# Kernel optimization log

Hardware: AMD Instinct MI355X
Metric: run time of the kernel (lower is better)

The kernel has to match this reference:

```python
import math
import jax, jax.numpy as jnp
import numpy as np

B, S, M, D, H, FF = 2, 2048, 64, 1024, 16, 4096
HD = D // H


def setup_inputs() -> dict:
    key = jax.random.key(0)
    ks = jax.random.split(key, 16)
    w = lambda k, shape: jax.random.normal(k, shape, dtype=jnp.float32) * 0.02
    # RoPE angles: theta_i = pos / 10000^(2i/head_dim)
    inv_freq = 1.0 / (10000.0 ** (jnp.arange(0, HD, 2, dtype=jnp.float32) / HD))
    ang = jnp.arange(S, dtype=jnp.float32)[:, None] * inv_freq[None, :]  # (S, HD//2)
    return {
        "tgt": jax.random.normal(ks[0], (B, S, D), dtype=jnp.float32),
        "memory": jax.random.normal(ks[1], (B, M, D), dtype=jnp.float32),
        "rope_cos": jnp.cos(ang),
        "rope_sin": jnp.sin(ang),
        "W_qkv": w(ks[2], (D, 3 * D)), "b_qkv": jnp.zeros((3 * D,), jnp.float32),
        "W_o": w(ks[3], (D, D)), "b_o": jnp.zeros((D,), jnp.float32),
        "Wq_c": w(ks[4], (D, D)), "bq_c": jnp.zeros((D,), jnp.float32),
        "Wk_c": w(ks[5], (D, D)), "bk_c": jnp.zeros((D,), jnp.float32),
        "Wv_c": w(ks[6], (D, D)), "bv_c": jnp.zeros((D,), jnp.float32),
        "W_co": w(ks[7], (D, D)), "b_co": jnp.zeros((D,), jnp.float32),
        "W1": w(ks[8], (D, FF)), "b1": jnp.zeros((FF,), jnp.float32),
        "W2": w(ks[9], (FF, D)), "b2": jnp.zeros((D,), jnp.float32),
        "g1": jnp.ones((D,), jnp.float32), "be1": jnp.zeros((D,), jnp.float32),
        "g2": jnp.ones((D,), jnp.float32), "be2": jnp.zeros((D,), jnp.float32),
        "g3": jnp.ones((D,), jnp.float32), "be3": jnp.zeros((D,), jnp.float32),
    }


def _layer_norm(x, g, b, eps=1e-5):
    mu = jnp.mean(x, axis=-1, keepdims=True)
    var = jnp.mean(jnp.square(x - mu), axis=-1, keepdims=True)
    return (x - mu) * jax.lax.rsqrt(var + eps) * g + b


def _apply_rope(x, cos, sin):
    # x: (B, H, S, HD); cos/sin: (S, HD//2). Pairs (even, odd) rotated as complex.
    xe, xo = x[..., 0::2], x[..., 1::2]
    c = cos[None, None]
    s = sin[None, None]
    re = xe * c - xo * s
    im = xe * s + xo * c
    return jnp.stack([re, im], axis=-1).reshape(x.shape)


def reference(tgt, memory, rope_cos, rope_sin, W_qkv, b_qkv, W_o, b_o,
              Wq_c, bq_c, Wk_c, bk_c, Wv_c, bv_c, W_co, b_co,
              W1, b1, W2, b2, g1, be1, g2, be2, g3, be3):
    b, s, d = tgt.shape
    scale = 1.0 / math.sqrt(HD)

    # --- RoPE self-attention (causal) ---
    x = _layer_norm(tgt, g1, be1)
    qkv = (x @ W_qkv + b_qkv).reshape(b, s, 3, H, HD)
    qkv = jnp.transpose(qkv, (2, 0, 3, 1, 4))  # (3, b, H, s, HD)
    q, k, v = qkv[0], qkv[1], qkv[2]
    q = _apply_rope(q, rope_cos[:s], rope_sin[:s])
    k = _apply_rope(k, rope_cos[:s], rope_sin[:s])
    attn = jnp.einsum('bhqd,bhkd->bhqk', q, k) * scale
    causal = jnp.tril(jnp.ones((s, s), dtype=bool))
    attn = jnp.where(causal[None, None], attn, -1e9)
    attn = jax.nn.softmax(attn, axis=-1)
    sa = jnp.einsum('bhqk,bhkd->bhqd', attn, v)
    sa = jnp.transpose(sa, (0, 2, 1, 3)).reshape(b, s, d)
    tgt = tgt + (sa @ W_o + b_o)

    # --- cross-attention to memory (no positional encoding) ---
    x = _layer_norm(tgt, g2, be2)
    m = memory.shape[1]
    qc = (x @ Wq_c + bq_c).reshape(b, s, H, HD).transpose(0, 2, 1, 3)
    kc = (memory @ Wk_c + bk_c).reshape(b, m, H, HD).transpose(0, 2, 1, 3)
    vc = (memory @ Wv_c + bv_c).reshape(b, m, H, HD).transpose(0, 2, 1, 3)
    ca = jax.nn.softmax(jnp.einsum('bhqd,bhkd->bhqk', qc, kc) * scale, axis=-1)
    co = jnp.einsum('bhqk,bhkd->bhqd', ca, vc)
    co = jnp.transpose(co, (0, 2, 1, 3)).reshape(b, s, d)
    tgt = tgt + (co @ W_co + b_co)

    # --- FFN (exact GELU, dropout disabled = eval) ---
    x = _layer_norm(tgt, g3, be3)
    ffn = jax.nn.gelu(x @ W1 + b1, approximate=False) @ W2 + b2
    return tgt + ffn
```

## Files before the change

### kernel.cpp

```cpp
#include <hip/hip_runtime.h>

typedef unsigned short u16;
typedef short bf16x8 __attribute__((ext_vector_type(8)));
typedef float f32x4 __attribute__((ext_vector_type(4)));

#define HN 16
#define SD 64
#define SEQ 2048
#define DM 1024
#define QSC 0.18033688f

__device__ __forceinline__ float bf2f(u16 h) {
  return __uint_as_float(((unsigned int)h) << 16);
}
__device__ __forceinline__ u16 f2bf(float f) {
  unsigned int x = __float_as_uint(f);
  x += 0x7fffu + ((x >> 16) & 1u);
  return (u16)(x >> 16);
}
__device__ __forceinline__ float geluf(float x) {
  return 0.5f * x * (1.0f + erff(x * 0.70710678118654752f));
}
__device__ __forceinline__ void load_lds16(const u16* g, u16* l) {
  __builtin_amdgcn_global_load_lds(
      (const __attribute__((address_space(1))) void*)g,
      (__attribute__((address_space(3))) void*)l, 16, 0, 0);
}

__global__ __launch_bounds__(256) void transpose_f2b(
    const float* __restrict__ in, u16* __restrict__ out, int K, int N) {
  __shared__ u16 T[64][72];
  const int n0 = blockIdx.x * 64, k0 = blockIdx.y * 64;
  const int tid = threadIdx.x;
#pragma unroll
  for (int it = 0; it < 2; ++it) {
    const int t = it * 256 + tid, r = t >> 3, c = (t & 7) * 8;
    const float* src = &in[(size_t)(k0 + r) * N + n0 + c];
    float4 d0 = *(const float4*)src;
    float4 d1 = *(const float4*)(src + 4);
    T[r][c + 0] = f2bf(d0.x);
    T[r][c + 1] = f2bf(d0.y);
    T[r][c + 2] = f2bf(d0.z);
    T[r][c + 3] = f2bf(d0.w);
    T[r][c + 4] = f2bf(d1.x);
    T[r][c + 5] = f2bf(d1.y);
    T[r][c + 6] = f2bf(d1.z);
    T[r][c + 7] = f2bf(d1.w);
  }
  __syncthreads();
#pragma unroll
  for (int it = 0; it < 2; ++it) {
    const int t = it * 256 + tid, r = t >> 3, c = (t & 7) * 8;
    uint4 d;
    u16* p = (u16*)&d;
#pragma unroll
    for (int j = 0; j < 8; ++j) p[j] = T[c + j][r];
    *(uint4*)&out[(size_t)(n0 + r) * K + k0 + c] = d;
  }
}

__global__ __launch_bounds__(256) void f2b_kernel(const float* __restrict__ in,
                                                  u16* __restrict__ out) {
  const int i = (blockIdx.x * 256 + threadIdx.x) * 4;
  float4 d = *(const float4*)&in[i];
  uint2 o;
  u16* po = (u16*)&o;
  po[0] = f2bf(d.x);
  po[1] = f2bf(d.y);
  po[2] = f2bf(d.z);
  po[3] = f2bf(d.w);
  *(uint2*)&out[i] = o;
}

__global__ __launch_bounds__(256) void ln_kernel(
    const float* __restrict__ x, const float* __restrict__ g,
    const float* __restrict__ be, u16* __restrict__ y) {
  const int row = blockIdx.x, tid = threadIdx.x;
  const float* xr = x + (size_t)row * DM;
  float4 d = *(const float4*)&xr[tid * 4];
  float v[4] = {d.x, d.y, d.z, d.w};
  float s1 = 0.f, s2 = 0.f;
#pragma unroll
  for (int j = 0; j < 4; ++j) {
    s1 += v[j];
    s2 += v[j] * v[j];
  }
#pragma unroll
  for (int dd = 1; dd < 64; dd <<= 1) {
    s1 += __shfl_xor(s1, dd, 64);
    s2 += __shfl_xor(s2, dd, 64);
  }
  __shared__ float p1[4], p2[4];
  const int lane = tid & 63, wv = tid >> 6;
  if (lane == 0) {
    p1[wv] = s1;
    p2[wv] = s2;
  }
  __syncthreads();
  s1 = p1[0] + p1[1] + p1[2] + p1[3];
  s2 = p2[0] + p2[1] + p2[2] + p2[3];
  const float mu = s1 * (1.f / DM);
  const float rs = rsqrtf(fmaxf(s2 * (1.f / DM) - mu * mu, 0.f) + 1e-5f);
  float4 gg = *(const float4*)&g[tid * 4];
  float4 bb = *(const float4*)&be[tid * 4];
  const float gv[4] = {gg.x, gg.y, gg.z, gg.w};
  const float bv[4] = {bb.x, bb.y, bb.z, bb.w};
  uint2 o;
  u16* po = (u16*)&o;
#pragma unroll
  for (int j = 0; j < 4; ++j) po[j] = f2bf((v[j] - mu) * rs * gv[j] + bv[j]);
  *(uint2*)&y[(size_t)row * DM + tid * 4] = o;
}

__global__ __launch_bounds__(256) void rope_kernel(
    u16* __restrict__ q, u16* __restrict__ k, const float* __restrict__ ct,
    const float* __restrict__ st) {
  const long long NG = 2LL * HN * SEQ * 8;
  long long gidx = (long long)blockIdx.x * 256 + threadIdx.x;
  const bool isq = (gidx < NG);
  u16* p = isq ? q : k;
  const float m = isq ? QSC : 1.0f;
  long long gg = isq ? gidx : gidx - NG;
  const int pib = (int)(gg & 7) * 4;
  const int s = (int)((gg >> 3) & (SEQ - 1));
  uint4 d = *(uint4*)&p[gg * 8];
  u16* e = (u16*)&d;
#pragma unroll
  for (int j = 0; j < 4; ++j) {
    const float c = ct[s * 32 + pib + j];
    const float sn = st[s * 32 + pib + j];
    const float xe = bf2f(e[2 * j]), xo = bf2f(e[2 * j + 1]);
    e[2 * j] = f2bf((xe * c - xo * sn) * m);
    e[2 * j + 1] = f2bf((xe * sn + xo * c) * m);
  }
  *(uint4*)&p[gg * 8] = d;
}

template <int EPI, int TM>
__global__ __launch_bounds__(256) void gemm_bt(
    const u16* __restrict__ A, const u16* __restrict__ Bt,
    const float* __restrict__ bias, const float* __restrict__ resid,
    void* __restrict__ C0, u16* __restrict__ C1, u16* __restrict__ C2, int M,
    int N, int K, int rpbl, float sc) {
  constexpr int MI = TM / 32;
  __shared__ __align__(16) u16 As[TM][64];
  __shared__ __align__(16) u16 Bs[128][64];
  const int tid = threadIdx.x;
  const int lane = tid & 63, wv = tid >> 6;
  const int l16 = lane & 15, quad = lane >> 4;

  int bx = blockIdx.x, by = blockIdx.y;
  const int gx = gridDim.x, gy = gridDim.y;
  if ((gy & 7) == 0) {
    const int f = by * gx + bx;
    const int c = f & 7, j = f >> 3;
    const int jm = j / gx;
    by = c * (gy >> 3) + jm;
    bx = j - jm * gx;
  }
  const int m0 = by * TM, n0 = bx * 128;
  const int wm = (wv >> 1) * (TM / 2), wn = (wv & 1) * 64;

  const int srow = lane >> 3;
  const int sblk = (lane & 7) ^ srow;
  const u16* ag[MI];
  const u16* bg[4];
  u16* la[MI];
  u16* lb[4];
#pragma unroll
  for (int i = 0; i < MI; ++i) {
    const int r0 = i * 32 + wv * 8;
    ag[i] = A + (size_t)(m0 + r0 + srow) * K + sblk * 8;
    la[i] = &As[r0][0] + lane * 8;
  }
#pragma unroll
  for (int i = 0; i < 4; ++i) {
    const int r0 = i * 32 + wv * 8;
    bg[i] = Bt + (size_t)(n0 + r0 + srow) * K + sblk * 8;
    lb[i] = &Bs[r0][0] + lane * 8;
  }

  f32x4 acc[MI][4] = {};

  for (int k0 = 0; k0 < K; k0 += 64) {
    __syncthreads();
#pragma unroll
    for (int i = 0; i < MI; ++i) load_lds16(ag[i] + k0, la[i]);
#pragma unroll
    for (int i = 0; i < 4; ++i) load_lds16(bg[i] + k0, lb[i]);
    __syncthreads();
#pragma unroll
    for (int kk = 0; kk < 2; ++kk) {
      bf16x8 af[MI], bfr[4];
#pragma unroll
      for (int mi = 0; mi < MI; ++mi) {
        const int row = wm + mi * 16 + l16;
        const int blk = (kk * 4 + quad) ^ (row & 7);
        af[mi] = *(const bf16x8*)&As[row][blk * 8];
      }
#pragma unroll
      for (int ni = 0; ni < 4; ++ni) {
        const int row = wn + ni * 16 + l16;
        const int blk = (kk * 4 + quad) ^ (row & 7);
        bfr[ni] = *(const bf16x8*)&Bs[row][blk * 8];
      }
#pragma unroll
      for (int mi = 0; mi < MI; ++mi)
#pragma unroll
        for (int ni = 0; ni < 4; ++ni)
          acc[mi][ni] = __builtin_amdgcn_mfma_f32_16x16x32_bf16(
              af[mi], bfr[ni], acc[mi][ni], 0, 0, 0);
    }
  }

  const int SL = 1 << rpbl;
#pragma unroll
  for (int mi = 0; mi < MI; ++mi) {
#pragma unroll
    for (int ni = 0; ni < 4; ++ni) {
#pragma unroll
      for (int r = 0; r < 4; ++r) {
        const int row = m0 + wm + mi * 16 + quad * 4 + r;
        const int col = n0 + wn + ni * 16 + l16;
        float vv = acc[mi][ni][r] + bias[col];
        if (EPI == 1) {
          vv += resid[(size_t)row * N + col];
          ((float*)C0)[(size_t)row * N + col] = vv;
        } else if (EPI == 2) {
          ((u16*)C0)[(size_t)row * N + col] = f2bf(geluf(vv));
        } else if (EPI == 3) {
          const int which = col >> 10;
          const int nn = col & 1023;
          const int h = nn >> 6, hd = nn & 63;
          const int b = row >> rpbl;
          const int s = row & (SL - 1);
          if (which == 2) {
            C2[(((size_t)b * HN + h) * SD + hd) * SL + s] = f2bf(vv);
          } else {
            u16* o = (which == 0) ? (u16*)C0 : C1;
            o[(((size_t)b * HN + h) * SL + s) * SD + hd] = f2bf(vv);
          }
        } else if (EPI == 4) {
          vv *= sc;
          const int h = col >> 6, hd = col & 63;
          const int b = row >> rpbl;
          const int s = row & (SL - 1);
          ((u16*)C0)[(((size_t)b * HN + h) * SL + s) * SD + hd] = f2bf(vv);
        } else if (EPI == 5) {
          const int h = col >> 6, hd = col & 63;
          const int b = row >> rpbl;
          const int s = row & (SL - 1);
          ((u16*)C0)[(((size_t)b * HN + h) * SD + hd) * SL + s] = f2bf(vv);
        } else {
          ((u16*)C0)[(size_t)row * N + col] = f2bf(vv);
        }
      }
    }
  }
}

template <int CAUSAL>
__global__ __launch_bounds__(512, 4) void attn_kernel(
    const u16* __restrict__ q, const u16* __restrict__ k,
    const u16* __restrict__ vt, u16* __restrict__ out, int kv_len) {
  __shared__ u16 Qs[128][72], Ks[64][72], VTs[64][72];
  __shared__ u16 Ps[128][68];
  const int tid = threadIdx.x;
  const int lane = tid & 63, wv = tid >> 6;
  const int t2 = wv >> 2, w4 = wv & 3;
  const int l16 = lane & 15, quad = lane >> 4;
  const int bx = blockIdx.x, bh = blockIdx.y;
  const int qtA = bx;
  const int qtB = CAUSAL ? (31 - bx) : (bx + 16);
  const int qt = t2 ? qtB : qtA;
  const u16* qb = q + (size_t)bh * SEQ * SD;
  const u16* kb = k + (size_t)bh * kv_len * SD;
  const u16* vtb = vt + (size_t)bh * SD * kv_len;

#pragma unroll
  for (int it = 0; it < 2; ++it) {
    const int t = it * 512 + tid, r = t >> 3, c = (t & 7) * 8;
    const int qrow = (r < 64) ? (qtA * 64 + r) : (qtB * 64 + (r - 64));
    *(uint4*)&Qs[r][c] = *(const uint4*)&qb[(size_t)qrow * SD + c];
  }

  f32x4 o_acc[4] = {};
  float l_i[4] = {};

  const int ktiles = CAUSAL ? (qtB + 1) : ((kv_len + 63) >> 6);
  const int sr = tid >> 3, sc8 = (tid & 7) * 8;

  for (int kt = 0; kt < ktiles; ++kt) {
    const uint4 kd = *(const uint4*)&kb[((size_t)kt * 64 + sr) * SD + sc8];
    const uint4 vd = *(const uint4*)&vtb[(size_t)sr * kv_len + kt * 64 + sc8];
    __syncthreads();
    *(uint4*)&Ks[sr][sc8] = kd;
    *(uint4*)&VTs[sr][sc8] = vd;
    __syncthreads();

    if (kt <= qt) {
      const int roff = t2 * 64 + w4 * 16;
      f32x4 s_acc[4] = {};
#pragma unroll
      for (int kk = 0; kk < 64; kk += 32) {
        const bf16x8 aq = *(const bf16x8*)&Qs[roff + l16][kk + quad * 8];
#pragma unroll
        for (int ni = 0; ni < 4; ++ni) {
          const bf16x8 bk = *(const bf16x8*)&Ks[ni * 16 + l16][kk + quad * 8];
          s_acc[ni] = __builtin_amdgcn_mfma_f32_16x16x32_bf16(aq, bk, s_acc[ni],
                                                              0, 0, 0);
        }
      }
      float rsum[4] = {0.f, 0.f, 0.f, 0.f};
      const bool dg = CAUSAL && (kt == qt);
#pragma unroll
      for (int ni = 0; ni < 4; ++ni)
#pragma unroll
        for (int r = 0; r < 4; ++r) {
          float sv = s_acc[ni][r];
          if (dg && (ni * 16 + l16 > w4 * 16 + quad * 4 + r)) sv = -1e9f;
          const float pe = __builtin_amdgcn_exp2f(sv);
          rsum[r] += pe;
          Ps[wv * 16 + quad * 4 + r][ni * 16 + l16] =
              (u16)(__float_as_uint(pe) >> 16);
        }
#pragma unroll
      for (int r = 0; r < 4; ++r) {
#pragma unroll
        for (int dd = 1; dd < 16; dd <<= 1)
          rsum[r] += __shfl_xor(rsum[r], dd, 64);
        l_i[r] += rsum[r];
      }
#pragma unroll
      for (int kk = 0; kk < 64; kk += 32) {
        const bf16x8 ap = *(const bf16x8*)&Ps[wv * 16 + l16][kk + quad * 8];
#pragma unroll
        for (int ni = 0; ni < 4; ++ni) {
          const bf16x8 bv = *(const bf16x8*)&VTs[ni * 16 + l16][kk + quad * 8];
          o_acc[ni] = __builtin_amdgcn_mfma_f32_16x16x32_bf16(ap, bv, o_acc[ni],
                                                              0, 0, 0);
        }
      }
    }
  }

  const int b = bh >> 4, h = bh & 15;
#pragma unroll
  for (int r = 0; r < 4; ++r) {
    const float inv = 1.f / l_i[r];
    const int s = qt * 64 + w4 * 16 + quad * 4 + r;
#pragma unroll
    for (int ni = 0; ni < 4; ++ni)
      out[((size_t)b * SEQ + s) * DM + h * SD + ni * 16 + l16] =
          f2bf(o_acc[ni][r] * inv);
  }
}

extern "C" void kernel_launch(void* const* d_in, const int* in_sizes, int n_in,
                              void* d_out, int out_size, void* d_ws,
                              size_t ws_size, hipStream_t stream) {
  (void)in_sizes;
  (void)n_in;
  (void)out_size;
  (void)ws_size;
  const float* tgt = (const float*)d_in[0];
  const float* mem = (const float*)d_in[1];
  const float* rc = (const float*)d_in[2];
  const float* rsn = (const float*)d_in[3];
  const float* W_qkv = (const float*)d_in[4];
  const float* b_qkv = (const float*)d_in[5];
  const float* W_o = (const float*)d_in[6];
  const float* b_o = (const float*)d_in[7];
  const float* Wq_c = (const float*)d_in[8];
  const float* bq_c = (const float*)d_in[9];
  const float* Wk_c = (const float*)d_in[10];
  const float* bk_c = (const float*)d_in[11];
  const float* Wv_c = (const float*)d_in[12];
  const float* bv_c = (const float*)d_in[13];
  const float* W_co = (const float*)d_in[14];
  const float* b_co = (const float*)d_in[15];
  const float* W1 = (const float*)d_in[16];
  const float* b1 = (const float*)d_in[17];
  const float* W2 = (const float*)d_in[18];
  const float* b2 = (const float*)d_in[19];
  const float* g1 = (const float*)d_in[20];
  const float* be1 = (const float*)d_in[21];
  const float* g2 = (const float*)d_in[22];
  const float* be2 = (const float*)d_in[23];
  const float* g3 = (const float*)d_in[24];
  const float* be3 = (const float*)d_in[25];

  const size_t M1 = 1048576;
  u16* w = (u16*)d_ws;
  u16* WTqkv = w;
  u16* WTo = w + 3 * M1;
  u16* WTqc = w + 4 * M1;
  u16* WTkc = w + 5 * M1;
  u16* WTvc = w + 6 * M1;
  u16* WTco = w + 7 * M1;
  u16* WT1 = w;
  u16* WT2 = w + 4 * M1;
  u16* xb = w + 8 * M1;
  u16* qb = w + 12 * M1;
  u16* kb = w + 16 * M1;
  u16* vbT = w + 20 * M1;
  u16* at = w + 24 * M1;
  u16* kc = w + 28 * M1;
  u16* vcT = kc + 131072;
  u16* memb = vcT + 131072;
  u16* ffh = qb;
  float* res = (float*)d_out;

  dim3 blk(256), blk512(512);
  transpose_f2b<<<dim3(48, 16), blk, 0, stream>>>(W_qkv, WTqkv, 1024, 3072);
  transpose_f2b<<<dim3(16, 16), blk, 0, stream>>>(W_o, WTo, 1024, 1024);
  transpose_f2b<<<dim3(16, 16), blk, 0, stream>>>(Wq_c, WTqc, 1024, 1024);
  transpose_f2b<<<dim3(16, 16), blk, 0, stream>>>(Wk_c, WTkc, 1024, 1024);
  transpose_f2b<<<dim3(16, 16), blk, 0, stream>>>(Wv_c, WTvc, 1024, 1024);
  transpose_f2b<<<dim3(16, 16), blk, 0, stream>>>(W_co, WTco, 1024, 1024);
  f2b_kernel<<<128, blk, 0, stream>>>(mem, memb);

  ln_kernel<<<4096, blk, 0, stream>>>(tgt, g1, be1, xb);
  gemm_bt<3, 128><<<dim3(24, 32), blk, 0, stream>>>(
      xb, WTqkv, b_qkv, nullptr, qb, kb, vbT, 4096, 3072, 1024, 11, 1.f);
  rope_kernel<<<4096, blk, 0, stream>>>(qb, kb, rc, rsn);
  attn_kernel<1><<<dim3(16, 32), blk512, 0, stream>>>(qb, kb, vbT, at, 2048);
  gemm_bt<1, 64><<<dim3(8, 64), blk, 0, stream>>>(
      at, WTo, b_o, tgt, res, nullptr, nullptr, 4096, 1024, 1024, 0, 1.f);
  ln_kernel<<<4096, blk, 0, stream>>>(res, g2, be2, xb);
  gemm_bt<4, 64><<<dim3(8, 64), blk, 0, stream>>>(
      xb, WTqc, bq_c, nullptr, qb, nullptr, nullptr, 4096, 1024, 1024, 11, QSC);
  gemm_bt<4, 64><<<dim3(8, 2), blk, 0, stream>>>(
      memb, WTkc, bk_c, nullptr, kc, nullptr, nullptr, 128, 1024, 1024, 6, 1.f);
  gemm_bt<5, 64><<<dim3(8, 2), blk, 0, stream>>>(
      memb, WTvc, bv_c, nullptr, vcT, nullptr, nullptr, 128, 1024, 1024, 6,
      1.f);
  attn_kernel<0><<<dim3(16, 32), blk512, 0, stream>>>(qb, kc, vcT, at, 64);
  gemm_bt<1, 64><<<dim3(8, 64), blk, 0, stream>>>(
      at, WTco, b_co, res, res, nullptr, nullptr, 4096, 1024, 1024, 0, 1.f);
  transpose_f2b<<<dim3(64, 16), blk, 0, stream>>>(W1, WT1, 1024, 4096);
  transpose_f2b<<<dim3(16, 64), blk, 0, stream>>>(W2, WT2, 4096, 1024);
  ln_kernel<<<4096, blk, 0, stream>>>(res, g3, be3, xb);
  gemm_bt<2, 128><<<dim3(32, 32), blk, 0, stream>>>(
      xb, WT1, b1, nullptr, ffh, nullptr, nullptr, 4096, 4096, 1024, 0, 1.f);
  gemm_bt<1, 64><<<dim3(8, 64), blk, 0, stream>>>(
      ffh, WT2, b2, res, res, nullptr, nullptr, 4096, 1024, 4096, 0, 1.f);
}
```

Measured before the change: 534.8 us.

## Fuse weight prep launches, RoPE into QKV epilogue, and split-KV attention

Merges the weight transposes and the memory conversion into two batched prep kernels. RoPE and the Q scale move into the QKV GEMM epilogue through a lane shuffle, which removes the separate rope pass over q and k. The cross-attention K and V projections now share one launch via blockIdx.z. Attention is restructured so each block handles one 64-row query tile, with its two wave groups splitting the KV tiles and merging partial results through LDS. The aim is fewer launches, less memory traffic and more blocks for attention, at the cost of extra LDS traffic and synchronisation for the merge.

```diff
diff --git a/kernel.cpp b/kernel.cpp
--- a/kernel.cpp
+++ b/kernel.cpp
@@ -27,11 +27,11 @@
       (__attribute__((address_space(3))) void*)l, 16, 0, 0);
 }
 
-__global__ __launch_bounds__(256) void transpose_f2b(
-    const float* __restrict__ in, u16* __restrict__ out, int K, int N) {
-  __shared__ u16 T[64][72];
-  const int n0 = blockIdx.x * 64, k0 = blockIdx.y * 64;
-  const int tid = threadIdx.x;
+__device__ __forceinline__ void trans_tile(const float* __restrict__ in,
+                                           u16* __restrict__ out, int K, int N,
+                                           int tx, int ty, int tid,
+                                           u16 (*T)[72]) {
+  const int n0 = tx * 64, k0 = ty * 64;
 #pragma unroll
   for (int it = 0; it < 2; ++it) {
     const int t = it * 256 + tid, r = t >> 3, c = (t & 7) * 8;
@@ -59,17 +59,54 @@
   }
 }
 
-__global__ __launch_bounds__(256) void f2b_kernel(const float* __restrict__ in,
-                                                  u16* __restrict__ out) {
-  const int i = (blockIdx.x * 256 + threadIdx.x) * 4;
-  float4 d = *(const float4*)&in[i];
+__global__ __launch_bounds__(256) void prep1(
+    const float* __restrict__ Wqkv, const float* __restrict__ Wo,
+    const float* __restrict__ Wqc, const float* __restrict__ Wkc,
+    const float* __restrict__ Wvc, const float* __restrict__ Wco,
+    u16* __restrict__ Tqkv, u16* __restrict__ To, u16* __restrict__ Tqc,
+    u16* __restrict__ Tkc, u16* __restrict__ Tvc, u16* __restrict__ Tco,
+    const float* __restrict__ mem, u16* __restrict__ memb) {
+  __shared__ u16 T[64][72];
+  const int t = blockIdx.x, tid = threadIdx.x;
+  if (t < 768) {
+    trans_tile(Wqkv, Tqkv, 1024, 3072, t % 48, t / 48, tid, T);
+    return;
+  }
+  if (t < 2048) {
+    const int u = t - 768, m = u >> 8, sub = u & 255;
+    const float* in;
+    u16* out;
+    if (m == 0) { in = Wo; out = To; }
+    else if (m == 1) { in = Wqc; out = Tqc; }
+    else if (m == 2) { in = Wkc; out = Tkc; }
+    else if (m == 3) { in = Wvc; out = Tvc; }
+    else { in = Wco; out = Tco; }
+    trans_tile(in, out, 1024, 1024, sub & 15, sub >> 4, tid, T);
+    return;
+  }
+  const int i = ((t - 2048) * 256 + tid) * 4;
+  float4 d = *(const float4*)&mem[i];
   uint2 o;
   u16* po = (u16*)&o;
   po[0] = f2bf(d.x);
   po[1] = f2bf(d.y);
   po[2] = f2bf(d.z);
   po[3] = f2bf(d.w);
-  *(uint2*)&out[i] = o;
+  *(uint2*)&memb[i] = o;
+}
+
+__global__ __launch_bounds__(256) void prep2(const float* __restrict__ W1,
+                                             const float* __restrict__ W2,
+                                             u16* __restrict__ T1,
+                                             u16* __restrict__ T2) {
+  __shared__ u16 T[64][72];
+  const int t = blockIdx.x, tid = threadIdx.x;
+  if (t < 1024) {
+    trans_tile(W1, T1, 1024, 4096, t & 63, t >> 6, tid, T);
+  } else {
+    const int u = t - 1024;
+    trans_tile(W2, T2, 4096, 1024, u & 15, u >> 4, tid, T);
+  }
 }
 
 __global__ __launch_bounds__(256) void ln_kernel(
@@ -112,42 +149,24 @@
   *(uint2*)&y[(size_t)row * DM + tid * 4] = o;
 }
 
-__global__ __launch_bounds__(256) void rope_kernel(
-    u16* __restrict__ q, u16* __restrict__ k, const float* __restrict__ ct,
-    const float* __restrict__ st) {
-  const long long NG = 2LL * HN * SEQ * 8;
-  long long gidx = (long long)blockIdx.x * 256 + threadIdx.x;
-  const bool isq = (gidx < NG);
-  u16* p = isq ? q : k;
-  const float m = isq ? QSC : 1.0f;
-  long long gg = isq ? gidx : gidx - NG;
-  const int pib = (int)(gg & 7) * 4;
-  const int s = (int)((gg >> 3) & (SEQ - 1));
-  uint4 d = *(uint4*)&p[gg * 8];
-  u16* e = (u16*)&d;
-#pragma unroll
-  for (int j = 0; j < 4; ++j) {
-    const float c = ct[s * 32 + pib + j];
-    const float sn = st[s * 32 + pib + j];
-    const float xe = bf2f(e[2 * j]), xo = bf2f(e[2 * j + 1]);
-    e[2 * j] = f2bf((xe * c - xo * sn) * m);
-    e[2 * j + 1] = f2bf((xe * sn + xo * c) * m);
-  }
-  *(uint4*)&p[gg * 8] = d;
-}
-
 template <int EPI, int TM>
 __global__ __launch_bounds__(256) void gemm_bt(
     const u16* __restrict__ A, const u16* __restrict__ Bt,
     const float* __restrict__ bias, const float* __restrict__ resid,
     void* __restrict__ C0, u16* __restrict__ C1, u16* __restrict__ C2, int M,
-    int N, int K, int rpbl, float sc) {
+    int N, int K, int rpbl, float sc, const float* __restrict__ rcos,
+    const float* __restrict__ rsin) {
   constexpr int MI = TM / 32;
   __shared__ __align__(16) u16 As[TM][64];
   __shared__ __align__(16) u16 Bs[128][64];
   const int tid = threadIdx.x;
   const int lane = tid & 63, wv = tid >> 6;
   const int l16 = lane & 15, quad = lane >> 4;
+
+  if (EPI == 6 && blockIdx.z) {
+    Bt = (const u16*)C1;
+    bias = resid;
+  }
 
   int bx = blockIdx.x, by = blockIdx.y;
   const int gx = gridDim.x, gy = gridDim.y;
@@ -229,6 +248,7 @@
         } else if (EPI == 2) {
           ((u16*)C0)[(size_t)row * N + col] = f2bf(geluf(vv));
         } else if (EPI == 3) {
+          const float partner = __shfl_xor(vv, 1);
           const int which = col >> 10;
           const int nn = col & 1023;
           const int h = nn >> 6, hd = nn & 63;
@@ -237,8 +257,14 @@
           if (which == 2) {
             C2[(((size_t)b * HN + h) * SD + hd) * SL + s] = f2bf(vv);
           } else {
-            u16* o = (which == 0) ? (u16*)C0 : C1;
-            o[(((size_t)b * HN + h) * SL + s) * SD + hd] = f2bf(vv);
+            const int p = hd >> 1;
+            const float cv = rcos[s * 32 + p];
+            const float sv2 = rsin[s * 32 + p];
+            float o = (hd & 1) ? (partner * sv2 + vv * cv)
+                               : (vv * cv - partner * sv2);
+            if (which == 0) o *= QSC;
+            u16* dst = (which == 0) ? (u16*)C0 : C1;
+            dst[(((size_t)b * HN + h) * SL + s) * SD + hd] = f2bf(o);
           }
         } else if (EPI == 4) {
           vv *= sc;
@@ -251,6 +277,14 @@
           const int b = row >> rpbl;
           const int s = row & (SL - 1);
           ((u16*)C0)[(((size_t)b * HN + h) * SD + hd) * SL + s] = f2bf(vv);
+        } else if (EPI == 6) {
+          const int h = col >> 6, hd = col & 63;
+          const int b = row >> rpbl;
+          const int s = row & (SL - 1);
+          if (blockIdx.z == 0)
+            ((u16*)C0)[(((size_t)b * HN + h) * SL + s) * SD + hd] = f2bf(vv);
+          else
+            C2[(((size_t)b * HN + h) * SD + hd) * SL + s] = f2bf(vv);
         } else {
           ((u16*)C0)[(size_t)row * N + col] = f2bf(vv);
         }
@@ -263,56 +297,68 @@
 __global__ __launch_bounds__(512, 4) void attn_kernel(
     const u16* __restrict__ q, const u16* __restrict__ k,
     const u16* __restrict__ vt, u16* __restrict__ out, int kv_len) {
-  __shared__ u16 Qs[128][72], Ks[64][72], VTs[64][72];
+  __shared__ u16 Qs[64][72];
+  __shared__ u16 Ks[128][72];
+  __shared__ u16 VTs[64][136];
   __shared__ u16 Ps[128][68];
   const int tid = threadIdx.x;
   const int lane = tid & 63, wv = tid >> 6;
   const int t2 = wv >> 2, w4 = wv & 3;
   const int l16 = lane & 15, quad = lane >> 4;
-  const int bx = blockIdx.x, bh = blockIdx.y;
-  const int qtA = bx;
-  const int qtB = CAUSAL ? (31 - bx) : (bx + 16);
-  const int qt = t2 ? qtB : qtA;
-  const u16* qb = q + (size_t)bh * SEQ * SD;
+  const int qt = blockIdx.x, bh = blockIdx.y;
+  const u16* qb = q + ((size_t)bh * SEQ + qt * 64) * SD;
   const u16* kb = k + (size_t)bh * kv_len * SD;
   const u16* vtb = vt + (size_t)bh * SD * kv_len;
 
-#pragma unroll
-  for (int it = 0; it < 2; ++it) {
-    const int t = it * 512 + tid, r = t >> 3, c = (t & 7) * 8;
-    const int qrow = (r < 64) ? (qtA * 64 + r) : (qtB * 64 + (r - 64));
-    *(uint4*)&Qs[r][c] = *(const uint4*)&qb[(size_t)qrow * SD + c];
+  {
+    const int r = tid >> 3, c = (tid & 7) * 8;
+    *(uint4*)&Qs[r][c] = *(const uint4*)&qb[(size_t)r * SD + c];
   }
 
   f32x4 o_acc[4] = {};
   float l_i[4] = {};
 
-  const int ktiles = CAUSAL ? (qtB + 1) : ((kv_len + 63) >> 6);
-  const int sr = tid >> 3, sc8 = (tid & 7) * 8;
-
-  for (int kt = 0; kt < ktiles; ++kt) {
-    const uint4 kd = *(const uint4*)&kb[((size_t)kt * 64 + sr) * SD + sc8];
-    const uint4 vd = *(const uint4*)&vtb[(size_t)sr * kv_len + kt * 64 + sc8];
+  const int nround =
+      CAUSAL ? ((qt >> 1) + 1) : ((kv_len + 127) >> 7);
+  const int kr = tid >> 2, kc4 = (tid & 3) * 16;
+  const int vr = tid >> 3, vc16 = (tid & 7) * 16;
+
+  for (int rd = 0; rd < nround; ++rd) {
+    const int c0 = rd << 7;
+    uint4 ka0 = {0, 0, 0, 0}, ka1 = {0, 0, 0, 0};
+    uint4 va0 = {0, 0, 0, 0}, va1 = {0, 0, 0, 0};
+    if (c0 + kr < kv_len) {
+      ka0 = *(const uint4*)&kb[(size_t)(c0 + kr) * SD + kc4];
+      ka1 = *(const uint4*)&kb[(size_t)(c0 + kr) * SD + kc4 + 8];
+    }
+    if (c0 + vc16 < kv_len) {
+      va0 = *(const uint4*)&vtb[(size_t)vr * kv_len + c0 + vc16];
+      va1 = *(const uint4*)&vtb[(size_t)vr * kv_len + c0 + vc16 + 8];
+    }
     __syncthreads();
-    *(uint4*)&Ks[sr][sc8] = kd;
-    *(uint4*)&VTs[sr][sc8] = vd;
+    *(uint4*)&Ks[kr][kc4] = ka0;
+    *(uint4*)&Ks[kr][kc4 + 8] = ka1;
+    *(uint4*)&VTs[vr][vc16] = va0;
+    *(uint4*)&VTs[vr][vc16 + 8] = va1;
     __syncthreads();
 
-    if (kt <= qt) {
-      const int roff = t2 * 64 + w4 * 16;
+    const int st = (rd << 1) + t2;
+    const bool part = CAUSAL ? (st <= qt) : (st * 64 < kv_len);
+    if (part) {
       f32x4 s_acc[4] = {};
 #pragma unroll
       for (int kk = 0; kk < 64; kk += 32) {
-        const bf16x8 aq = *(const bf16x8*)&Qs[roff + l16][kk + quad * 8];
+        const bf16x8 aq = *(const bf16x8*)&Qs[w4 * 16 + l16][kk + quad * 8];
 #pragma unroll
         for (int ni = 0; ni < 4; ++ni) {
-          const bf16x8 bk = *(const bf16x8*)&Ks[ni * 16 + l16][kk + quad * 8];
+          const bf16x8 bk =
+              *(const bf16x8*)&Ks[t2 * 64 + ni * 16 + l16][kk + quad * 8];
           s_acc[ni] = __builtin_amdgcn_mfma_f32_16x16x32_bf16(aq, bk, s_acc[ni],
                                                               0, 0, 0);
         }
       }
       float rsum[4] = {0.f, 0.f, 0.f, 0.f};
-      const bool dg = CAUSAL && (kt == qt);
+      const bool dg = CAUSAL && (st == qt);
 #pragma unroll
       for (int ni = 0; ni < 4; ++ni)
 #pragma unroll
@@ -336,7 +382,8 @@
         const bf16x8 ap = *(const bf16x8*)&Ps[wv * 16 + l16][kk + quad * 8];
 #pragma unroll
         for (int ni = 0; ni < 4; ++ni) {
-          const bf16x8 bv = *(const bf16x8*)&VTs[ni * 16 + l16][kk + quad * 8];
+          const bf16x8 bv =
+              *(const bf16x8*)&VTs[ni * 16 + l16][t2 * 64 + kk + quad * 8];
           o_acc[ni] = __builtin_amdgcn_mfma_f32_16x16x32_bf16(ap, bv, o_acc[ni],
                                                               0, 0, 0);
         }
@@ -344,15 +391,34 @@
     }
   }
 
-  const int b = bh >> 4, h = bh & 15;
-#pragma unroll
-  for (int r = 0; r < 4; ++r) {
-    const float inv = 1.f / l_i[r];
-    const int s = qt * 64 + w4 * 16 + quad * 4 + r;
-#pragma unroll
-    for (int ni = 0; ni < 4; ++ni)
-      out[((size_t)b * SEQ + s) * DM + h * SD + ni * 16 + l16] =
-          f2bf(o_acc[ni][r] * inv);
+  __syncthreads();
+  float* Omb = (float*)&Ks[0][0];
+  float* lbuf = (float*)&VTs[0][0];
+  if (t2 == 1) {
+#pragma unroll
+    for (int r = 0; r < 4; ++r) {
+      const int row = w4 * 16 + quad * 4 + r;
+      if (l16 == 0) lbuf[row] = l_i[r];
+#pragma unroll
+      for (int ni = 0; ni < 4; ++ni)
+        Omb[row * 68 + ni * 16 + l16] = o_acc[ni][r];
+    }
+  }
+  __syncthreads();
+  if (t2 == 0) {
+    const int b = bh >> 4, h = bh & 15;
+#pragma unroll
+    for (int r = 0; r < 4; ++r) {
+      const int row = w4 * 16 + quad * 4 + r;
+      const float inv = 1.f / (l_i[r] + lbuf[row]);
+      const int s = qt * 64 + row;
+#pragma unroll
+      for (int ni = 0; ni < 4; ++ni) {
+        const float val = o_acc[ni][r] + Omb[row * 68 + ni * 16 + l16];
+        out[((size_t)b * SEQ + s) * DM + h * SD + ni * 16 + l16] =
+            f2bf(val * inv);
+      }
+    }
   }
 }
 
@@ -412,37 +478,37 @@
   float* res = (float*)d_out;
 
   dim3 blk(256), blk512(512);
-  transpose_f2b<<<dim3(48, 16), blk, 0, stream>>>(W_qkv, WTqkv, 1024, 3072);
-  transpose_f2b<<<dim3(16, 16), blk, 0, stream>>>(W_o, WTo, 1024, 1024);
-  transpose_f2b<<<dim3(16, 16), blk, 0, stream>>>(Wq_c, WTqc, 1024, 1024);
-  transpose_f2b<<<dim3(16, 16), blk, 0, stream>>>(Wk_c, WTkc, 1024, 1024);
-  transpose_f2b<<<dim3(16, 16), blk, 0, stream>>>(Wv_c, WTvc, 1024, 1024);
-  transpose_f2b<<<dim3(16, 16), blk, 0, stream>>>(W_co, WTco, 1024, 1024);
-  f2b_kernel<<<128, blk, 0, stream>>>(mem, memb);
+  prep1<<<2176, blk, 0, stream>>>(W_qkv, W_o, Wq_c, Wk_c, Wv_c, W_co, WTqkv,
+                                  WTo, WTqc, WTkc, WTvc, WTco, mem, memb);
 
   ln_kernel<<<4096, blk, 0, stream>>>(tgt, g1, be1, xb);
   gemm_bt<3, 128><<<dim3(24, 32), blk, 0, stream>>>(
-      xb, WTqkv, b_qkv, nullptr, qb, kb, vbT, 4096, 3072, 1024, 11, 1.f);
-  rope_kernel<<<4096, blk, 0, stream>>>(qb, kb, rc, rsn);
-  attn_kernel<1><<<dim3(16, 32), blk512, 0, stream>>>(qb, kb, vbT, at, 2048);
-  gemm_bt<1, 64><<<dim3(8, 64), blk, 0, stream>>>(
-      at, WTo, b_o, tgt, res, nullptr, nullptr, 4096, 1024, 1024, 0, 1.f);
+      xb, WTqkv, b_qkv, nullptr, qb, kb, vbT, 4096, 3072, 1024, 11, 1.f, rc,
+      rsn);
+  attn_kernel<1><<<dim3(32, 32), blk512, 0, stream>>>(qb, kb, vbT, at, 2048);
+  gemm_bt<1, 64><<<dim3(8, 64), blk, 0, stream>>>(at, WTo, b_o, tgt, res,
+                                                  nullptr, nullptr, 4096, 1024,
+                                                  1024, 0, 1.f, nullptr,
+                                                  nullptr);
   ln_kernel<<<4096, blk, 0, stream>>>(res, g2, be2, xb);
   gemm_bt<4, 64><<<dim3(8, 64), blk, 0, stream>>>(
-      xb, WTqc, bq_c, nullptr, qb, nullptr, nullptr, 4096, 1024, 1024, 11, QSC);
-  gemm_bt<4, 64><<<dim3(8, 2), blk, 0, stream>>>(
-      memb, WTkc, bk_c, nullptr, kc, nullptr, nullptr, 128, 1024, 1024, 6, 1.f);
-  gemm_bt<5, 64><<<dim3(8, 2), blk, 0, stream>>>(
-      memb, WTvc, bv_c, nullptr, vcT, nullptr, nullptr, 128, 1024, 1024, 6,
-      1.f);
-  attn_kernel<0><<<dim3(16, 32), blk512, 0, stream>>>(qb, kc, vcT, at, 64);
-  gemm_bt<1, 64><<<dim3(8, 64), blk, 0, stream>>>(
-      at, WTco, b_co, res, res, nullptr, nullptr, 4096, 1024, 1024, 0, 1.f);
-  transpose_f2b<<<dim3(64, 16), blk, 0, stream>>>(W1, WT1, 1024, 4096);
-  transpose_f2b<<<dim3(16, 64), blk, 0, stream>>>(W2, WT2, 4096, 1024);
+      xb, WTqc, bq_c, nullptr, qb, nullptr, nullptr, 4096, 1024, 1024, 11, QSC,
+      nullptr, nullptr);
+  gemm_bt<6, 64><<<dim3(8, 2, 2), blk, 0, stream>>>(
+      memb, WTkc, bk_c, bv_c, kc, WTvc, vcT, 128, 1024, 1024, 6, 1.f, nullptr,
+      nullptr);
+  attn_kernel<0><<<dim3(32, 32), blk512, 0, stream>>>(qb, kc, vcT, at, 64);
+  gemm_bt<1, 64><<<dim3(8, 64), blk, 0, stream>>>(at, WTco, b_co, res, res,
+                                                  nullptr, nullptr, 4096, 1024,
+                                                  1024, 0, 1.f, nullptr,
+                                                  nullptr);
+  prep2<<<2048, blk, 0, stream>>>(W1, W2, WT1, WT2);
   ln_kernel<<<4096, blk, 0, stream>>>(res, g3, be3, xb);
   gemm_bt<2, 128><<<dim3(32, 32), blk, 0, stream>>>(
-      xb, WT1, b1, nullptr, ffh, nullptr, nullptr, 4096, 4096, 1024, 0, 1.f);
-  gemm_bt<1, 64><<<dim3(8, 64), blk, 0, stream>>>(
-      ffh, WT2, b2, res, res, nullptr, nullptr, 4096, 1024, 4096, 0, 1.f);
-}
+      xb, WT1, b1, nullptr, ffh, nullptr, nullptr, 4096, 4096, 1024, 0, 1.f,
+      nullptr, nullptr);
+  gemm_bt<1, 64><<<dim3(8, 64), blk, 0, stream>>>(ffh, WT2, b2, res, res,
+                                                  nullptr, nullptr, 4096, 1024,
+                                                  4096, 0, 1.f, nullptr,
+                                                  nullptr);
+}
```

Result: slower. 548.1 us (+2.5%).
